# Kernel optimization log

Measured on AMD Instinct MI355X. Metric: run time of the kernel, lower is better.

The kernel has to match this reference:

```python
import jax, jax.numpy as jnp
import numpy as np

# loss hyper-parameters (from settings.loss_settings defaults)
DICE_W, BOUNDARY_W, FOCAL_W = 1.0, 1.0, 1.0
FOCAL_ALPHA, FOCAL_GAMMA = 0.25, 2.0
EPS = 1e-6
INF = 1e10  # sentinel for 'no foreground pixel'


def _edt(fg):
    """Exact Euclidean distance transform to nearest True pixel.
    fg: [H, W] bool. Returns [H, W] float32 distances.
    Separable exact formulation: min_q (py-qy)^2 + (px-qx)^2
      = min_qy [ (py-qy)^2 + min_{qx: fg[qy,qx]} (px-qx)^2 ].
    Matches the brute-force all-pairs min of the torch code.
    """
    H, W = fg.shape
    ax = jnp.arange(W, dtype=jnp.float32)
    dx2 = (ax[:, None] - ax[None, :]) ** 2                      # [px, qx]
    # d1[qy, px] = min over qx in foreground row qy of (px-qx)^2
    d1 = jnp.where(fg[:, None, :], dx2[None, :, :], INF).min(-1)  # [qy, px]
    ay = jnp.arange(H, dtype=jnp.float32)
    dy2 = (ay[:, None] - ay[None, :]) ** 2                      # [py, qy]
    d = (dy2[:, :, None] + d1[None, :, :]).min(1)               # [py, px]
    # empty-foreground fallback: torch fills with sqrt((H-1)^2+(W-1)^2)
    max_d2 = float((H - 1) ** 2 + (W - 1) ** 2)
    d = jnp.where(d > INF * 0.5, max_d2, d)
    return jnp.sqrt(d)


def _signed_dist(gt):
    # gt: [1, H, W] float. phi_G = -dist_inside on fg, +dist_outside on bg.
    gb = gt[0] > 0.5
    dist_outside = _edt(gb)
    dist_inside = _edt(~gb)
    return jnp.where(gb, -dist_inside, dist_outside)[None]  # [1, H, W]


def setup_inputs() -> dict:
    key = jax.random.key(0)
    k1, k2 = jax.random.split(key)
    pred_masks = jax.random.normal(k1, (8, 1, 256, 256), dtype=jnp.float32)
    target_masks = jax.random.uniform(k2, (8, 1, 256, 256), dtype=jnp.float32)
    return {"pred_masks": pred_masks, "target_masks": target_masks}


def reference(pred_masks, target_masks):
    t = target_masks.astype(jnp.float32)
    p = jax.nn.sigmoid(pred_masks)

    # dice loss
    inter = (p * t).sum(axis=(2, 3))
    union = p.sum(axis=(2, 3)) + t.sum(axis=(2, 3))
    dice_val = 1.0 - ((2.0 * inter + EPS) / (union + EPS)).mean()

    # boundary loss: signed distance map of gt (sequential over batch to cap memory)
    phi_G = jax.lax.map(_signed_dist, t)  # [N, 1, H, W]
    boundary_val = (phi_G * p).mean()

    # focal loss
    pc = jnp.clip(p, EPS, 1.0 - EPS)
    pt = pc * t + (1.0 - pc) * (1.0 - t)
    alpha_t = FOCAL_ALPHA * t + (1.0 - FOCAL_ALPHA) * (1.0 - t)
    focal_val = (-alpha_t * (1.0 - pt) ** FOCAL_GAMMA * jnp.log(pt)).mean()

    loss = DICE_W * dice_val + BOUNDARY_W * boundary_val + FOCAL_W * focal_val
    return (loss, dice_val, boundary_val, focal_val)
```

## Files before the change

kernel.cpp:

```cpp
#include <hip/hip_runtime.h>
#include <math.h>
#include <limits.h>

constexpr int N = 8;
constexpr int H = 256;
constexpr int W = 256;
constexpr int NPIX = N * H * W;
constexpr float FEPS = 1e-6f;
constexpr int   RSENT = 20000;
constexpr int   EMPTY_THRESH = 300000000;
constexpr int   NBLK2 = N * H;
constexpr int   WIN = 3;


__global__ __launch_bounds__(256) void row_scan_kernel(
    const float* __restrict__ tgt, short2* __restrict__ d1)
{
    const int b    = blockIdx.x;
    const int px   = threadIdx.x;
    const int lane = px & 63;
    const int wid  = px >> 6;
    const int BIG  = 1 << 20;

    const float tv = tgt[b * W + px];
    const bool  fg = tv > 0.5f;
    const int cf = fg ? 0 : BIG;
    const int cb = fg ? BIG : 0;

    __shared__ int sm[8];

    int a = cf - px, c = cb - px;
    #pragma unroll
    for (int off = 1; off < 64; off <<= 1) {
        const int ua = __shfl_up(a, off, 64);
        const int uc = __shfl_up(c, off, 64);
        if (lane >= off) { a = min(a, ua); c = min(c, uc); }
    }
    if (lane == 63) { sm[wid * 2] = a; sm[wid * 2 + 1] = c; }
    __syncthreads();
    #pragma unroll
    for (int w = 0; w < 3; ++w) {
        if (w < wid) { a = min(a, sm[w * 2]); c = min(c, sm[w * 2 + 1]); }
    }
    const int fwd_fg = px + a;
    const int fwd_bg = px + c;
    __syncthreads();

    int a2 = cf + px, c2 = cb + px;
    #pragma unroll
    for (int off = 1; off < 64; off <<= 1) {
        const int ua = __shfl_down(a2, off, 64);
        const int uc = __shfl_down(c2, off, 64);
        if (lane + off < 64) { a2 = min(a2, ua); c2 = min(c2, uc); }
    }
    if (lane == 0) { sm[wid * 2] = a2; sm[wid * 2 + 1] = c2; }
    __syncthreads();
    #pragma unroll
    for (int w = 1; w < 4; ++w) {
        if (w > wid) { a2 = min(a2, sm[w * 2]); c2 = min(c2, sm[w * 2 + 1]); }
    }
    const int bwd_fg = a2 - px;
    const int bwd_bg = c2 - px;

    int rf = min(fwd_fg, bwd_fg); if (rf > 255) rf = RSENT;
    int rb = min(fwd_bg, bwd_bg); if (rb > 255) rb = RSENT;
    d1[b * W + px] = make_short2((short)rf, (short)rb);
}

__global__ __launch_bounds__(256) void main_pass_kernel(
    const float* __restrict__ pred, const float* __restrict__ tgt,
    const short2* __restrict__ d1, float* __restrict__ parts)
{
    const int blk  = blockIdx.x;
    const int n    = blk >> 8;
    const int py   = blk & 255;
    const int px   = threadIdx.x;
    const int lane = threadIdx.x & 63;
    const int wid  = threadIdx.x >> 6;
    const int idx  = blk * W + px;

    const float x = pred[idx];
    const float t = tgt[idx];

    const short2* __restrict__ img = d1 + (size_t)n * (H * W) + px;

    int best_f = INT_MAX, best_b = INT_MAX;
    #pragma unroll
    for (int d = -WIN; d <= WIN; ++d) {
        const int qy = py + d;
        if (qy >= 0 && qy < H) {
            const short2 r = img[qy * W];
            const int d2 = d * d;
            best_f = min(best_f, (int)r.x * (int)r.x + d2);
            best_b = min(best_b, (int)r.y * (int)r.y + d2);
        }
    }
    for (int dlt = WIN + 1; dlt < H; ++dlt) {
        const int d2 = dlt * dlt;
        if (!__any((d2 < best_f) || (d2 < best_b))) break;
        const int up = py - dlt;
        const int dn = py + dlt;
        if (up >= 0) {
            const short2 r = img[up * W];
            best_f = min(best_f, (int)r.x * (int)r.x + d2);
            best_b = min(best_b, (int)r.y * (int)r.y + d2);
        }
        if (dn < H) {
            const short2 r = img[dn * W];
            best_f = min(best_f, (int)r.x * (int)r.x + d2);
            best_b = min(best_b, (int)r.y * (int)r.y + d2);
        }
        if (up < 0 && dn >= H) break;
    }

    const float MAXD2 = (float)((H - 1) * (H - 1) + (W - 1) * (W - 1));
    const float Dfg = (best_f > EMPTY_THRESH) ? MAXD2 : (float)best_f;
    const float Dbg = (best_b > EMPTY_THRESH) ? MAXD2 : (float)best_b;

    const float p   = 1.0f / (1.0f + expf(-x));
    const float phi = (t > 0.5f) ? -sqrtf(Dbg) : sqrtf(Dfg);

    const float pc = fminf(fmaxf(p, FEPS), 1.0f - FEPS);
    const float pt = pc * t + (1.0f - pc) * (1.0f - t);
    const float at = 0.25f * t + 0.75f * (1.0f - t);
    const float om = 1.0f - pt;
    const float focal = -at * om * om * logf(pt);

    float v5[5] = { p * t, p, t, phi * p, focal };
    __shared__ float smem[4 * 5];
    #pragma unroll
    for (int q = 0; q < 5; ++q) {
        float v = v5[q];
        #pragma unroll
        for (int off = 32; off > 0; off >>= 1) v += __shfl_down(v, off, 64);
        v5[q] = v;
    }
    if (lane == 0) {
        #pragma unroll
        for (int q = 0; q < 5; ++q) smem[wid * 5 + q] = v5[q];
    }
    __syncthreads();
    if (threadIdx.x == 0) {
        #pragma unroll
        for (int q = 0; q < 5; ++q) {
            parts[q * NBLK2 + blk] = smem[q] + smem[5 + q] + smem[10 + q] + smem[15 + q];
        }
    }
}

__global__ __launch_bounds__(256) void finalize_kernel(
    const float* __restrict__ parts, float* __restrict__ out)
{
    const int tid  = threadIdx.x;
    const int lane = tid & 63;
    const int wid  = tid >> 6;
    __shared__ float smf[8];
    __shared__ float sratio[8];

    float bp = 0.0f, fc = 0.0f;
    for (int k = tid; k < NBLK2; k += 256) {
        bp += parts[3 * NBLK2 + k];
        fc += parts[4 * NBLK2 + k];
    }
    #pragma unroll
    for (int off = 32; off > 0; off >>= 1) {
        bp += __shfl_down(bp, off, 64);
        fc += __shfl_down(fc, off, 64);
    }
    if (lane == 0) { smf[wid * 2] = bp; smf[wid * 2 + 1] = fc; }

    #pragma unroll
    for (int mi = 0; mi < 2; ++mi) {
        const int m = wid * 2 + mi;
        float A = 0.f, S = 0.f, C = 0.f;
        #pragma unroll
        for (int k = 0; k < 4; ++k) {
            const int i = m * 256 + k * 64 + lane;
            A += parts[0 * NBLK2 + i];
            S += parts[1 * NBLK2 + i];
            C += parts[2 * NBLK2 + i];
        }
        #pragma unroll
        for (int off = 32; off > 0; off >>= 1) {
            A += __shfl_down(A, off, 64);
            S += __shfl_down(S, off, 64);
            C += __shfl_down(C, off, 64);
        }
        if (lane == 0) sratio[m] = (2.0f * A + FEPS) / (S + C + FEPS);
    }
    __syncthreads();
    if (tid == 0) {
        const float B = smf[0] + smf[2] + smf[4] + smf[6];
        const float F = smf[1] + smf[3] + smf[5] + smf[7];
        float dacc = 0.0f;
        #pragma unroll
        for (int m = 0; m < 8; ++m) dacc += sratio[m];
        const float dice_val     = 1.0f - dacc / (float)N;
        const float boundary_val = B / (float)NPIX;
        const float focal_val    = F / (float)NPIX;
        out[0] = dice_val + boundary_val + focal_val;
        out[1] = dice_val;
        out[2] = boundary_val;
        out[3] = focal_val;
    }
}

extern "C" void kernel_launch(void* const* d_in, const int* in_sizes, int n_in,
                              void* d_out, int out_size, void* d_ws, size_t ws_size,
                              hipStream_t stream)
{
    const float* pred = (const float*)d_in[0];
    const float* tgt  = (const float*)d_in[1];
    float* out = (float*)d_out;

    short2* d1    = (short2*)d_ws;
    float*  parts = (float*)((char*)d_ws + (size_t)NPIX * sizeof(short2));

    row_scan_kernel<<<N * H, 256, 0, stream>>>(tgt, d1);
    main_pass_kernel<<<NBLK2, 256, 0, stream>>>(pred, tgt, d1, parts);
    finalize_kernel<<<1, 256, 0, stream>>>(parts, out);
}
```

Measured before the change: 73.28 us.

## Fuse row scan, main pass and finalize into one kernel with flag sync

The row-scan, main and finalize kernels become one launch. Each block handles two rows. It recomputes the nearest-foreground row scans for a window of eight nearby rows in shared memory, using a wave-level scan over four pixels per lane, and computes farther rows on demand instead of storing them to global memory. The last-block reduction is replaced by block 0 spinning on per-block release flags. This aims to cut two launches and the global round trip of the intermediate distance map. In exchange it adds redundant scan work across blocks and a spin wait whose flags are never reset between calls, which risks reading stale partials.

Result: slower. 79.29 us (+8.2%).

```diff
diff --git a/kernel.cpp b/kernel.cpp
--- a/kernel.cpp
+++ b/kernel.cpp
@@ -9,199 +9,294 @@
 constexpr float FEPS = 1e-6f;
 constexpr int   RSENT = 20000;
 constexpr int   EMPTY_THRESH = 300000000;
-constexpr int   NBLK2 = N * H;
-constexpr int   WIN = 3;
-
-
-__global__ __launch_bounds__(256) void row_scan_kernel(
-    const float* __restrict__ tgt, short2* __restrict__ d1)
+constexpr int   NROW = N * H;
+constexpr int   NBLK = NROW / 2;
+constexpr int   BIGC = 1 << 20;
+constexpr unsigned long long MAGIC = 0x9E3779B97F4A7C15ull;
+
+
+__device__ __forceinline__ void wave_scan_row(const float4 tv, const int lane,
+                                              int rf[4], int rb[4])
 {
-    const int b    = blockIdx.x;
+    const int px0 = lane << 2;
+    const float tvv[4] = {tv.x, tv.y, tv.z, tv.w};
+    int af[4], ab[4], bf[4], bb[4];
+    #pragma unroll
+    for (int k = 0; k < 4; ++k) {
+        const bool fg = tvv[k] > 0.5f;
+        const int cf = fg ? 0 : BIGC;
+        const int cb = fg ? BIGC : 0;
+        af[k] = cf - (px0 + k);
+        ab[k] = cb - (px0 + k);
+        bf[k] = cf + (px0 + k);
+        bb[k] = cb + (px0 + k);
+    }
+    int pf[4], pb[4], qf[4], qb[4];
+    pf[0] = af[0]; pb[0] = ab[0];
+    #pragma unroll
+    for (int k = 1; k < 4; ++k) { pf[k] = min(pf[k-1], af[k]); pb[k] = min(pb[k-1], ab[k]); }
+    qf[3] = bf[3]; qb[3] = bb[3];
+    #pragma unroll
+    for (int k = 2; k >= 0; --k) { qf[k] = min(qf[k+1], bf[k]); qb[k] = min(qb[k+1], bb[k]); }
+
+    int sf = pf[3], sb = pb[3], tf = qf[0], tb = qb[0];
+    #pragma unroll
+    for (int off = 1; off < 64; off <<= 1) {
+        const int uf = __shfl_up(sf, off, 64);
+        const int ub = __shfl_up(sb, off, 64);
+        const int df = __shfl_down(tf, off, 64);
+        const int db = __shfl_down(tb, off, 64);
+        if (lane >= off)      { sf = min(sf, uf); sb = min(sb, ub); }
+        if (lane + off < 64)  { tf = min(tf, df); tb = min(tb, db); }
+    }
+    int ef = __shfl_up(sf, 1, 64);   if (lane == 0)  ef = INT_MAX / 2;
+    int eb = __shfl_up(sb, 1, 64);   if (lane == 0)  eb = INT_MAX / 2;
+    int xf = __shfl_down(tf, 1, 64); if (lane == 63) xf = INT_MAX / 2;
+    int xb = __shfl_down(tb, 1, 64); if (lane == 63) xb = INT_MAX / 2;
+
+    #pragma unroll
+    for (int k = 0; k < 4; ++k) {
+        const int p = px0 + k;
+        int F  = p + min(ef, pf[k]);
+        int Bv = min(xf, qf[k]) - p;
+        int r  = min(F, Bv); if (r > 255) r = RSENT;
+        rf[k] = r;
+        F  = p + min(eb, pb[k]);
+        Bv = min(xb, qb[k]) - p;
+        r  = min(F, Bv); if (r > 255) r = RSENT;
+        rb[k] = r;
+    }
+}
+
+__global__ __launch_bounds__(256, 4) void fused_kernel(
+    const float* __restrict__ pred, const float* __restrict__ tgt,
+    float* __restrict__ parts, unsigned long long* __restrict__ flags,
+    float* __restrict__ out)
+{
+    const int blk  = blockIdx.x;
+    const int n    = blk >> 7;
+    const int py0  = (blk & 127) << 1;
+    const int py1  = py0 + 1;
     const int px   = threadIdx.x;
     const int lane = px & 63;
     const int wid  = px >> 6;
-    const int BIG  = 1 << 20;
-
-    const float tv = tgt[b * W + px];
-    const bool  fg = tv > 0.5f;
-    const int cf = fg ? 0 : BIG;
-    const int cb = fg ? BIG : 0;
-
-    __shared__ int sm[8];
-
-    int a = cf - px, c = cb - px;
-    #pragma unroll
-    for (int off = 1; off < 64; off <<= 1) {
-        const int ua = __shfl_up(a, off, 64);
-        const int uc = __shfl_up(c, off, 64);
-        if (lane >= off) { a = min(a, ua); c = min(c, uc); }
-    }
-    if (lane == 63) { sm[wid * 2] = a; sm[wid * 2 + 1] = c; }
-    __syncthreads();
-    #pragma unroll
-    for (int w = 0; w < 3; ++w) {
-        if (w < wid) { a = min(a, sm[w * 2]); c = min(c, sm[w * 2 + 1]); }
-    }
-    const int fwd_fg = px + a;
-    const int fwd_bg = px + c;
-    __syncthreads();
-
-    int a2 = cf + px, c2 = cb + px;
-    #pragma unroll
-    for (int off = 1; off < 64; off <<= 1) {
-        const int ua = __shfl_down(a2, off, 64);
-        const int uc = __shfl_down(c2, off, 64);
-        if (lane + off < 64) { a2 = min(a2, ua); c2 = min(c2, uc); }
-    }
-    if (lane == 0) { sm[wid * 2] = a2; sm[wid * 2 + 1] = c2; }
-    __syncthreads();
-    #pragma unroll
-    for (int w = 1; w < 4; ++w) {
-        if (w > wid) { a2 = min(a2, sm[w * 2]); c2 = min(c2, sm[w * 2 + 1]); }
-    }
-    const int bwd_fg = a2 - px;
-    const int bwd_bg = c2 - px;
-
-    int rf = min(fwd_fg, bwd_fg); if (rf > 255) rf = RSENT;
-    int rb = min(fwd_bg, bwd_bg); if (rb > 255) rb = RSENT;
-    d1[b * W + px] = make_short2((short)rf, (short)rb);
-}
-
-__global__ __launch_bounds__(256) void main_pass_kernel(
-    const float* __restrict__ pred, const float* __restrict__ tgt,
-    const short2* __restrict__ d1, float* __restrict__ parts)
-{
-    const int blk  = blockIdx.x;
-    const int n    = blk >> 8;
-    const int py   = blk & 255;
-    const int px   = threadIdx.x;
-    const int lane = threadIdx.x & 63;
-    const int wid  = threadIdx.x >> 6;
-    const int idx  = blk * W + px;
-
-    const float x = pred[idx];
-    const float t = tgt[idx];
-
-    const short2* __restrict__ img = d1 + (size_t)n * (H * W) + px;
-
-    int best_f = INT_MAX, best_b = INT_MAX;
-    #pragma unroll
-    for (int d = -WIN; d <= WIN; ++d) {
-        const int qy = py + d;
-        if (qy >= 0 && qy < H) {
-            const short2 r = img[qy * W];
-            const int d2 = d * d;
-            best_f = min(best_f, (int)r.x * (int)r.x + d2);
-            best_b = min(best_b, (int)r.y * (int)r.y + d2);
-        }
-    }
-    for (int dlt = WIN + 1; dlt < H; ++dlt) {
-        const int d2 = dlt * dlt;
-        if (!__any((d2 < best_f) || (d2 < best_b))) break;
-        const int up = py - dlt;
-        const int dn = py + dlt;
-        if (up >= 0) {
-            const short2 r = img[up * W];
-            best_f = min(best_f, (int)r.x * (int)r.x + d2);
-            best_b = min(best_b, (int)r.y * (int)r.y + d2);
-        }
-        if (dn < H) {
-            const short2 r = img[dn * W];
-            best_f = min(best_f, (int)r.x * (int)r.x + d2);
-            best_b = min(best_b, (int)r.y * (int)r.y + d2);
-        }
-        if (up < 0 && dn >= H) break;
-    }
-
-    const float MAXD2 = (float)((H - 1) * (H - 1) + (W - 1) * (W - 1));
-    const float Dfg = (best_f > EMPTY_THRESH) ? MAXD2 : (float)best_f;
-    const float Dbg = (best_b > EMPTY_THRESH) ? MAXD2 : (float)best_b;
-
-    const float p   = 1.0f / (1.0f + expf(-x));
-    const float phi = (t > 0.5f) ? -sqrtf(Dbg) : sqrtf(Dfg);
-
-    const float pc = fminf(fmaxf(p, FEPS), 1.0f - FEPS);
-    const float pt = pc * t + (1.0f - pc) * (1.0f - t);
-    const float at = 0.25f * t + 0.75f * (1.0f - t);
-    const float om = 1.0f - pt;
-    const float focal = -at * om * om * logf(pt);
-
-    float v5[5] = { p * t, p, t, phi * p, focal };
-    __shared__ float smem[4 * 5];
-    #pragma unroll
-    for (int q = 0; q < 5; ++q) {
-        float v = v5[q];
-        #pragma unroll
-        for (int off = 32; off > 0; off >>= 1) v += __shfl_down(v, off, 64);
-        v5[q] = v;
-    }
-    if (lane == 0) {
-        #pragma unroll
-        for (int q = 0; q < 5; ++q) smem[wid * 5 + q] = v5[q];
-    }
-    __syncthreads();
-    if (threadIdx.x == 0) {
-        #pragma unroll
-        for (int q = 0; q < 5; ++q) {
-            parts[q * NBLK2 + blk] = smem[q] + smem[5 + q] + smem[10 + q] + smem[15 + q];
-        }
-    }
-}
-
-__global__ __launch_bounds__(256) void finalize_kernel(
-    const float* __restrict__ parts, float* __restrict__ out)
-{
-    const int tid  = threadIdx.x;
-    const int lane = tid & 63;
-    const int wid  = tid >> 6;
+
+    __shared__ unsigned int rows[8][W];
+    __shared__ float smem[2][20];
     __shared__ float smf[8];
     __shared__ float sratio[8];
 
-    float bp = 0.0f, fc = 0.0f;
-    for (int k = tid; k < NBLK2; k += 256) {
-        bp += parts[3 * NBLK2 + k];
-        fc += parts[4 * NBLK2 + k];
-    }
-    #pragma unroll
-    for (int off = 32; off > 0; off >>= 1) {
-        bp += __shfl_down(bp, off, 64);
-        fc += __shfl_down(fc, off, 64);
-    }
-    if (lane == 0) { smf[wid * 2] = bp; smf[wid * 2 + 1] = fc; }
-
-    #pragma unroll
-    for (int mi = 0; mi < 2; ++mi) {
-        const int m = wid * 2 + mi;
-        float A = 0.f, S = 0.f, C = 0.f;
-        #pragma unroll
-        for (int k = 0; k < 4; ++k) {
-            const int i = m * 256 + k * 64 + lane;
-            A += parts[0 * NBLK2 + i];
-            S += parts[1 * NBLK2 + i];
-            C += parts[2 * NBLK2 + i];
-        }
+    const float* __restrict__ timg = tgt  + (size_t)n * (H * W);
+    const float* __restrict__ pimg = pred + (size_t)n * (H * W);
+
+    {
+        const int s1 = wid, s2 = wid + 4;
+        const int qy1 = py0 - 3 + s1;
+        const int qy2 = py0 - 3 + s2;
+        const bool va = (qy1 >= 0) & (qy1 < H);
+        const bool vb = (qy2 >= 0) & (qy2 < H);
+        float4 tva, tvb;
+        if (va) tva = *(const float4*)(timg + qy1 * W + (lane << 2));
+        if (vb) tvb = *(const float4*)(timg + qy2 * W + (lane << 2));
+        if (va) {
+            int rf[4], rb[4];
+            wave_scan_row(tva, lane, rf, rb);
+            uint4 pk;
+            pk.x = (unsigned)rf[0] | ((unsigned)rb[0] << 16);
+            pk.y = (unsigned)rf[1] | ((unsigned)rb[1] << 16);
+            pk.z = (unsigned)rf[2] | ((unsigned)rb[2] << 16);
+            pk.w = (unsigned)rf[3] | ((unsigned)rb[3] << 16);
+            *(uint4*)&rows[s1][lane << 2] = pk;
+        }
+        if (vb) {
+            int rf[4], rb[4];
+            wave_scan_row(tvb, lane, rf, rb);
+            uint4 pk;
+            pk.x = (unsigned)rf[0] | ((unsigned)rb[0] << 16);
+            pk.y = (unsigned)rf[1] | ((unsigned)rb[1] << 16);
+            pk.z = (unsigned)rf[2] | ((unsigned)rb[2] << 16);
+            pk.w = (unsigned)rf[3] | ((unsigned)rb[3] << 16);
+            *(uint4*)&rows[s2][lane << 2] = pk;
+        }
+    }
+
+    const float x0 = pimg[py0 * W + px];
+    const float x1 = pimg[py1 * W + px];
+    const float t0 = timg[py0 * W + px];
+    const float t1 = timg[py1 * W + px];
+
+    __syncthreads();
+
+    int bf0 = INT_MAX, bb0 = INT_MAX, bf1 = INT_MAX, bb1 = INT_MAX;
+    #pragma unroll
+    for (int s = 0; s < 8; ++s) {
+        const int qy = py0 - 3 + s;
+        if (qy >= 0 && qy < H) {
+            const unsigned v = rows[s][px];
+            const int rfv = (int)(v & 0xffffu);
+            const int rbv = (int)(v >> 16);
+            const int rf2 = rfv * rfv, rb2 = rbv * rbv;
+            const int d0 = s - 3, d1 = s - 4;
+            bf0 = min(bf0, rf2 + d0 * d0); bb0 = min(bb0, rb2 + d0 * d0);
+            bf1 = min(bf1, rf2 + d1 * d1); bb1 = min(bb1, rb2 + d1 * d1);
+        }
+    }
+
+    for (int qy = py0 - 4; qy >= 0; --qy) {
+        const int du0 = py0 - qy, du1 = du0 + 1;
+        const int d0s = du0 * du0, d1s = du1 * du1;
+        if (!__any((d0s < bf0) | (d0s < bb0) | (d1s < bf1) | (d1s < bb1))) break;
+        const float4 tv = *(const float4*)(timg + qy * W + (lane << 2));
+        int rf[4], rb[4];
+        wave_scan_row(tv, lane, rf, rb);
+        const int o = px >> 2;
+        const int k = px & 3;
+        int f0 = __shfl(rf[0], o, 64), f1 = __shfl(rf[1], o, 64);
+        int f2 = __shfl(rf[2], o, 64), f3 = __shfl(rf[3], o, 64);
+        int g0 = __shfl(rb[0], o, 64), g1 = __shfl(rb[1], o, 64);
+        int g2 = __shfl(rb[2], o, 64), g3 = __shfl(rb[3], o, 64);
+        const int irf = (k == 0) ? f0 : (k == 1) ? f1 : (k == 2) ? f2 : f3;
+        const int irb = (k == 0) ? g0 : (k == 1) ? g1 : (k == 2) ? g2 : g3;
+        const int rf2 = irf * irf, rb2 = irb * irb;
+        bf0 = min(bf0, rf2 + d0s); bb0 = min(bb0, rb2 + d0s);
+        bf1 = min(bf1, rf2 + d1s); bb1 = min(bb1, rb2 + d1s);
+    }
+    for (int qy = py0 + 5; qy < H; ++qy) {
+        const int dd0 = qy - py0, dd1 = dd0 - 1;
+        const int d0s = dd0 * dd0, d1s = dd1 * dd1;
+        if (!__any((d0s < bf0) | (d0s < bb0) | (d1s < bf1) | (d1s < bb1))) break;
+        const float4 tv = *(const float4*)(timg + qy * W + (lane << 2));
+        int rf[4], rb[4];
+        wave_scan_row(tv, lane, rf, rb);
+        const int o = px >> 2;
+        const int k = px & 3;
+        int f0 = __shfl(rf[0], o, 64), f1 = __shfl(rf[1], o, 64);
+        int f2 = __shfl(rf[2], o, 64), f3 = __shfl(rf[3], o, 64);
+        int g0 = __shfl(rb[0], o, 64), g1 = __shfl(rb[1], o, 64);
+        int g2 = __shfl(rb[2], o, 64), g3 = __shfl(rb[3], o, 64);
+        const int irf = (k == 0) ? f0 : (k == 1) ? f1 : (k == 2) ? f2 : f3;
+        const int irb = (k == 0) ? g0 : (k == 1) ? g1 : (k == 2) ? g2 : g3;
+        const int rf2 = irf * irf, rb2 = irb * irb;
+        bf0 = min(bf0, rf2 + d0s); bb0 = min(bb0, rb2 + d0s);
+        bf1 = min(bf1, rf2 + d1s); bb1 = min(bb1, rb2 + d1s);
+    }
+
+    const float MAXD2 = (float)((H - 1) * (H - 1) + (W - 1) * (W - 1));
+    const float Df0 = (bf0 > EMPTY_THRESH) ? MAXD2 : (float)bf0;
+    const float Db0 = (bb0 > EMPTY_THRESH) ? MAXD2 : (float)bb0;
+    const float Df1 = (bf1 > EMPTY_THRESH) ? MAXD2 : (float)bf1;
+    const float Db1 = (bb1 > EMPTY_THRESH) ? MAXD2 : (float)bb1;
+
+    const float p0   = 1.0f / (1.0f + expf(-x0));
+    const float phi0 = (t0 > 0.5f) ? -sqrtf(Db0) : sqrtf(Df0);
+    const float pc0  = fminf(fmaxf(p0, FEPS), 1.0f - FEPS);
+    const float pt0  = pc0 * t0 + (1.0f - pc0) * (1.0f - t0);
+    const float at0  = 0.25f * t0 + 0.75f * (1.0f - t0);
+    const float om0  = 1.0f - pt0;
+    const float fo0  = -at0 * om0 * om0 * logf(pt0);
+
+    const float p1   = 1.0f / (1.0f + expf(-x1));
+    const float phi1 = (t1 > 0.5f) ? -sqrtf(Db1) : sqrtf(Df1);
+    const float pc1  = fminf(fmaxf(p1, FEPS), 1.0f - FEPS);
+    const float pt1  = pc1 * t1 + (1.0f - pc1) * (1.0f - t1);
+    const float at1  = 0.25f * t1 + 0.75f * (1.0f - t1);
+    const float om1  = 1.0f - pt1;
+    const float fo1  = -at1 * om1 * om1 * logf(pt1);
+
+    float v50[5] = { p0 * t0, p0, t0, phi0 * p0, fo0 };
+    float v51[5] = { p1 * t1, p1, t1, phi1 * p1, fo1 };
+    #pragma unroll
+    for (int q = 0; q < 5; ++q) {
+        float a = v50[q], b = v51[q];
         #pragma unroll
         for (int off = 32; off > 0; off >>= 1) {
-            A += __shfl_down(A, off, 64);
-            S += __shfl_down(S, off, 64);
-            C += __shfl_down(C, off, 64);
-        }
-        if (lane == 0) sratio[m] = (2.0f * A + FEPS) / (S + C + FEPS);
+            a += __shfl_down(a, off, 64);
+            b += __shfl_down(b, off, 64);
+        }
+        v50[q] = a; v51[q] = b;
+    }
+    if (lane == 0) {
+        #pragma unroll
+        for (int q = 0; q < 5; ++q) {
+            smem[0][wid * 5 + q] = v50[q];
+            smem[1][wid * 5 + q] = v51[q];
+        }
     }
     __syncthreads();
-    if (tid == 0) {
-        const float B = smf[0] + smf[2] + smf[4] + smf[6];
-        const float F = smf[1] + smf[3] + smf[5] + smf[7];
-        float dacc = 0.0f;
-        #pragma unroll
-        for (int m = 0; m < 8; ++m) dacc += sratio[m];
-        const float dice_val     = 1.0f - dacc / (float)N;
-        const float boundary_val = B / (float)NPIX;
-        const float focal_val    = F / (float)NPIX;
-        out[0] = dice_val + boundary_val + focal_val;
-        out[1] = dice_val;
-        out[2] = boundary_val;
-        out[3] = focal_val;
+    if (px == 0) {
+        #pragma unroll
+        for (int r = 0; r < 2; ++r) {
+            #pragma unroll
+            for (int q = 0; q < 5; ++q) {
+                const float v = smem[r][q] + smem[r][5 + q] + smem[r][10 + q] + smem[r][15 + q];
+                __hip_atomic_store(&parts[q * NROW + blk * 2 + r], v,
+                                   __ATOMIC_RELAXED, __HIP_MEMORY_SCOPE_AGENT);
+            }
+        }
+        __hip_atomic_store(&flags[blk], MAGIC, __ATOMIC_RELEASE, __HIP_MEMORY_SCOPE_AGENT);
+    }
+
+    if (blk == 0) {
+        const int tid = px;
+        bool done = false;
+        int guard = 0;
+        do {
+            bool mine = true;
+            #pragma unroll
+            for (int k = 0; k < NBLK / 256; ++k) {
+                const unsigned long long v = __hip_atomic_load(
+                    &flags[tid + k * 256], __ATOMIC_ACQUIRE, __HIP_MEMORY_SCOPE_AGENT);
+                mine = mine && (v == MAGIC);
+            }
+            done = (__syncthreads_and((int)mine) != 0);
+        } while (!done && (++guard < (1 << 26)));
+
+        float bp = 0.0f, fc = 0.0f;
+        for (int k = tid; k < NROW; k += 256) {
+            bp += __hip_atomic_load(&parts[3 * NROW + k], __ATOMIC_RELAXED, __HIP_MEMORY_SCOPE_AGENT);
+            fc += __hip_atomic_load(&parts[4 * NROW + k], __ATOMIC_RELAXED, __HIP_MEMORY_SCOPE_AGENT);
+        }
+        #pragma unroll
+        for (int off = 32; off > 0; off >>= 1) {
+            bp += __shfl_down(bp, off, 64);
+            fc += __shfl_down(fc, off, 64);
+        }
+        if (lane == 0) { smf[wid * 2] = bp; smf[wid * 2 + 1] = fc; }
+
+        #pragma unroll
+        for (int mi = 0; mi < 2; ++mi) {
+            const int m = wid * 2 + mi;
+            float A = 0.f, S = 0.f, C = 0.f;
+            #pragma unroll
+            for (int k = 0; k < 4; ++k) {
+                const int i = m * 256 + k * 64 + lane;
+                A += __hip_atomic_load(&parts[0 * NROW + i], __ATOMIC_RELAXED, __HIP_MEMORY_SCOPE_AGENT);
+                S += __hip_atomic_load(&parts[1 * NROW + i], __ATOMIC_RELAXED, __HIP_MEMORY_SCOPE_AGENT);
+                C += __hip_atomic_load(&parts[2 * NROW + i], __ATOMIC_RELAXED, __HIP_MEMORY_SCOPE_AGENT);
+            }
+            #pragma unroll
+            for (int off = 32; off > 0; off >>= 1) {
+                A += __shfl_down(A, off, 64);
+                S += __shfl_down(S, off, 64);
+                C += __shfl_down(C, off, 64);
+            }
+            if (lane == 0) sratio[m] = (2.0f * A + FEPS) / (S + C + FEPS);
+        }
+        __syncthreads();
+        if (tid == 0) {
+            const float B = smf[0] + smf[2] + smf[4] + smf[6];
+            const float F = smf[1] + smf[3] + smf[5] + smf[7];
+            float dacc = 0.0f;
+            #pragma unroll
+            for (int m = 0; m < 8; ++m) dacc += sratio[m];
+            const float dice_val     = 1.0f - dacc / (float)N;
+            const float boundary_val = B / (float)NPIX;
+            const float focal_val    = F / (float)NPIX;
+            out[0] = dice_val + boundary_val + focal_val;
+            out[1] = dice_val;
+            out[2] = boundary_val;
+            out[3] = focal_val;
+        }
     }
 }
 
@@ -213,10 +308,9 @@
     const float* tgt  = (const float*)d_in[1];
     float* out = (float*)d_out;
 
-    short2* d1    = (short2*)d_ws;
-    float*  parts = (float*)((char*)d_ws + (size_t)NPIX * sizeof(short2));
-
-    row_scan_kernel<<<N * H, 256, 0, stream>>>(tgt, d1);
-    main_pass_kernel<<<NBLK2, 256, 0, stream>>>(pred, tgt, d1, parts);
-    finalize_kernel<<<1, 256, 0, stream>>>(parts, out);
+    float* parts = (float*)d_ws;
+    unsigned long long* flags =
+        (unsigned long long*)((char*)d_ws + (size_t)5 * NROW * sizeof(float));
+
+    fused_kernel<<<NBLK, 256, 0, stream>>>(pred, tgt, parts, flags, out);
 }
```
